# Performance work log

Measured on AMD Instinct MI355X. Metric: run time of the kernel, lower is better.

## Reference

```python
import jax, jax.numpy as jnp
import numpy as np

C_IN = 512


def _rms(h, gamma):
    # F.normalize(x, dim=1) * sqrt(C) * gamma  (channel_first, h: [b, c, l])
    c = h.shape[1]
    n = jnp.sqrt(jnp.sum(h * h, axis=1, keepdims=True))
    return h / jnp.maximum(n, 1e-12) * (c ** 0.5) * gamma[None, :, None]


def _pw(w, b, h):
    # 1x1 conv == pointwise linear over channel dim; h: [b, c, l]
    return jnp.einsum('oc,bcl->bol', w, h) + b[None, :, None]


def setup_inputs() -> dict:
    key = jax.random.key(0)
    ks = jax.random.split(key, 10)
    B, C, T, H, W = 1, C_IN, 16, 32, 32
    inp = {'x': jax.random.normal(ks[0], (B, C, T, H, W), jnp.float32)}
    names = ['qs', 'ks', 'vs', 'ps', 'qt', 'kt', 'vt', 'pt']
    for i, n in enumerate(names):
        inp[n + '_w'] = jax.random.normal(ks[i + 1], (C, C), jnp.float32) * 0.02
        inp[n + '_b'] = jnp.zeros((C,), jnp.float32)
    inp['norm_s_gamma'] = jnp.ones((C,), jnp.float32)
    inp['norm_t_gamma'] = jnp.ones((C,), jnp.float32)
    inp['max_temporal_window'] = 8
    return inp


def reference(x, qs_w, qs_b, ks_w, ks_b, vs_w, vs_b, ps_w, ps_b,
              qt_w, qt_b, kt_w, kt_b, vt_w, vt_b, pt_w, pt_b,
              norm_s_gamma, norm_t_gamma, max_temporal_window):
    B, C, T, H, W = x.shape
    scale = C ** -0.5

    # ---- spatial attention: (b t) c (h w) ----
    xs = x.transpose(0, 2, 1, 3, 4).reshape(B * T, C, H * W)
    h = _rms(xs, norm_s_gamma)
    q = _pw(qs_w, qs_b, h)
    k = _pw(ks_w, ks_b, h)
    v = _pw(vs_w, vs_b, h)
    scores = jnp.einsum('bcl,bcm->blm', q, k) * scale  # [bt, HW, HW]
    attn = jax.nn.softmax(scores, axis=-1)
    o = jnp.einsum('bcm,blm->bcl', v, attn)
    xs = xs + _pw(ps_w, ps_b, o)
    x = xs.reshape(B, T, C, H, W).transpose(0, 2, 1, 3, 4)

    # ---- temporal attention: (b h w) c t, causal + bounded window ----
    xt = x.transpose(0, 3, 4, 1, 2).reshape(B * H * W, C, T)
    h = _rms(xt, norm_t_gamma)
    q = _pw(qt_w, qt_b, h)
    k = _pw(kt_w, kt_b, h)
    v = _pw(vt_w, vt_b, h)
    scores = jnp.einsum('bcl,bcm->blm', q, k) * scale  # [bhw, T, T]
    i = jnp.arange(T)[:, None]
    j = jnp.arange(T)[None, :]
    allowed = j <= i  # causal
    if max_temporal_window is not None and max_temporal_window > 0:
        allowed = allowed & (i - j < max_temporal_window)  # sliding window
    mask = jnp.where(allowed, 0.0, jnp.finfo(scores.dtype).min)
    attn = jax.nn.softmax(scores + mask[None], axis=-1)
    o = jnp.einsum('bcm,blm->bcl', v, attn)
    xt = xt + _pw(pt_w, pt_b, o)
    x = xt.reshape(B, H, W, C, T).transpose(0, 3, 4, 1, 2)
    return x
```

## Files before the change

### kernel.cpp

```cpp
#include <hip/hip_runtime.h>

typedef __attribute__((ext_vector_type(8))) short bf16x8;
typedef __attribute__((ext_vector_type(4))) float f32x4;

__device__ __forceinline__ short f2bf(float f) {
  union { float f; unsigned u; } a; a.f = f;
  unsigned r = a.u + 0x7fffu + ((a.u >> 16) & 1u);
  return (short)(r >> 16);
}
__device__ __forceinline__ float bf2f(short s) {
  union { unsigned u; float f; } a;
  a.u = ((unsigned)(unsigned short)s) << 16; return a.f;
}
__device__ __forceinline__ float blo(unsigned u) { union { unsigned u; float f; } a; a.u = u << 16; return a.f; }
__device__ __forceinline__ float bhi(unsigned u) { union { unsigned u; float f; } a; a.u = u & 0xffff0000u; return a.f; }
__device__ __forceinline__ unsigned packbf(float lo, float hi) {
  return (unsigned)(unsigned short)f2bf(lo) | ((unsigned)(unsigned short)f2bf(hi) << 16);
}
__device__ __forceinline__ void ldscp16(const void* g, void* l) {
  __builtin_amdgcn_global_load_lds((const __attribute__((address_space(1))) void*)g,
                                   (__attribute__((address_space(3))) void*)l, 16, 0, 0);
}
__device__ __forceinline__ void stv(float* p, float v) { *p = v; }
__device__ __forceinline__ void stv(short* p, float v) { *p = f2bf(v); }

__global__ __launch_bounds__(256) void setup_all(
    const float* __restrict__ w0, const float* __restrict__ w1,
    const float* __restrict__ w2, const float* __restrict__ w3,
    const float* __restrict__ w4, const float* __restrict__ w5,
    const float* __restrict__ w6, const float* __restrict__ w7,
    const float* __restrict__ g_s, const float* __restrict__ g_t,
    short* __restrict__ Wb, float* __restrict__ zs,
    const float* __restrict__ qs_b, const float* __restrict__ vs_b,
    const float* __restrict__ ps_b, const float* __restrict__ qt_b,
    const float* __restrict__ vt_b, const float* __restrict__ pt_b,
    float* __restrict__ bt_s, float* __restrict__ bt_t,
    float* __restrict__ wus, float* __restrict__ wut) {
  const int bid = blockIdx.x, tid = threadIdx.x;
  if (bid < 8192) {
    int idx = bid * 256 + tid;
    const float* ws[8] = {w0, w1, w2, w3, w4, w5, w6, w7};
    int wi = idx >> 18, loc = idx & 262143;
    int r = loc >> 9, q = loc & 511;
    float v, g;
    if (wi == 3 || wi == 7) { v = ws[wi][loc]; g = 1.f; }
    else {
      v = ws[wi][q * 512 + r];
      g = (wi <= 2) ? g_s[r] : g_t[r];
    }
    Wb[idx] = f2bf(v * g);
  } else if (bid < 8512) {
    zs[(bid - 8192) * 256 + tid] = 0.f;
  } else {
    const int w = tid >> 6, lane = tid & 63;
    const int b = (bid - 8512) * 4 + w;
    float s = 0.f;
    if (b < 1024) {
      const bool sp = b < 512;
      const float* W = sp ? w3 : w7;
      const float* vb = sp ? vs_b : vt_b;
      const int r = b & 511;
#pragma unroll
      for (int c = lane; c < 512; c += 64) s += W[r * 512 + c] * vb[c];
#pragma unroll
      for (int off = 32; off > 0; off >>= 1) s += __shfl_xor(s, off);
      if (lane == 0) (sp ? bt_s : bt_t)[r] = s + (sp ? ps_b : pt_b)[r];
    } else {
      const bool sp = b < 1536;
      const float* W = sp ? w1 : w5;
      const float* qb = sp ? qs_b : qt_b;
      const int c = b & 511;
#pragma unroll
      for (int o = lane; o < 512; o += 64) s += W[o * 512 + c] * qb[o];
#pragma unroll
      for (int off = 32; off > 0; off >>= 1) s += __shfl_xor(s, off);
      if (lane == 0)
        (sp ? wus : wut)[c] = s * (sp ? g_s[c] : g_t[c]);
    }
  }
}

__global__ __launch_bounds__(256) void txp_sumsq(
    const float* __restrict__ src, short* __restrict__ dst,
    short* __restrict__ xb, float* __restrict__ ss,
    const float* __restrict__ wu, float* __restrict__ us) {
  constexpr long N = 16384;
  __shared__ short T[64][66];
  __shared__ float part[16][16][4];
  __shared__ float part2[16][16][4];
  const int tid = threadIdx.x;
  const long n0 = (long)blockIdx.x * 64;
  const int c0 = blockIdx.y * 64;
  const int n4 = (tid & 15) * 4;
  float s0 = 0.f, s1 = 0.f, s2 = 0.f, s3 = 0.f;
  float u0 = 0.f, u1 = 0.f, u2 = 0.f, u3 = 0.f;
#pragma unroll
  for (int i = 0; i < 4; ++i) {
    int cl = i * 16 + (tid >> 4);
    float4 v = *(const float4*)&src[(long)(c0 + cl) * N + n0 + n4];
    float wc = wu[c0 + cl];
    s0 += v.x * v.x; s1 += v.y * v.y; s2 += v.z * v.z; s3 += v.w * v.w;
    u0 += wc * v.x; u1 += wc * v.y; u2 += wc * v.z; u3 += wc * v.w;
    short e0 = f2bf(v.x), e1 = f2bf(v.y), e2 = f2bf(v.z), e3 = f2bf(v.w);
    T[n4 + 0][cl] = e0; T[n4 + 1][cl] = e1;
    T[n4 + 2][cl] = e2; T[n4 + 3][cl] = e3;
    uint2 o;
    o.x = (unsigned)(unsigned short)e0 | ((unsigned)(unsigned short)e1 << 16);
    o.y = (unsigned)(unsigned short)e2 | ((unsigned)(unsigned short)e3 << 16);
    *(uint2*)&xb[(long)(c0 + cl) * N + n0 + n4] = o;
  }
  part[tid >> 4][tid & 15][0] = s0; part[tid >> 4][tid & 15][1] = s1;
  part[tid >> 4][tid & 15][2] = s2; part[tid >> 4][tid & 15][3] = s3;
  part2[tid >> 4][tid & 15][0] = u0; part2[tid >> 4][tid & 15][1] = u1;
  part2[tid >> 4][tid & 15][2] = u2; part2[tid >> 4][tid & 15][3] = u3;
  __syncthreads();
  if (tid < 64) {
    float s = 0.f, u = 0.f;
#pragma unroll
    for (int cg = 0; cg < 16; ++cg) {
      s += part[cg][tid >> 2][tid & 3];
      u += part2[cg][tid >> 2][tid & 3];
    }
    atomicAdd(&ss[n0 + tid], s);
    atomicAdd(&us[n0 + tid], u);
  }
#pragma unroll
  for (int p = 0; p < 4; ++p) {
    int nl = p * 16 + (tid >> 4);
    int cl = (tid & 15) * 4;
    uint2 o;
    o.x = (unsigned)(unsigned short)T[nl][cl] |
          ((unsigned)(unsigned short)T[nl][cl + 1] << 16);
    o.y = (unsigned)(unsigned short)T[nl][cl + 2] |
          ((unsigned)(unsigned short)T[nl][cl + 3] << 16);
    *(uint2*)&dst[(n0 + nl) * 512 + c0 + cl] = o;
  }
}

template <typename OutT, int BIAS_MODE, int SCALE_MODE, int RESID_MODE, int EPI,
          int BM = 128, int FOLD = 0, int BK = 64>
__global__ __launch_bounds__(256, (BM == 128 && BK == 64) ? 3 : 2) void gemm_nt(
    const short* __restrict__ A, const short* __restrict__ B,
    OutT* __restrict__ D, const float* __restrict__ bias,
    const float* __restrict__ ssv, const float* __restrict__ uvec,
    float* __restrict__ rs, float* __restrict__ rs2,
    const float* __restrict__ wvec,
    const float* __restrict__ residf, const short* __restrict__ residb,
    int K, int lda, int ldb, int ldd,
    long aBatch, long bBatch, long dBatch, long sBatch, float scale) {
  constexpr int WR = BM / 64;
  constexpr int WC = 4 / WR;
  constexpr int NW = (128 / WC) / 16;
  constexpr int CH = BK / 8;
  constexpr int MSK = CH - 1;
  constexpr int RPR = 256 / CH;
  __shared__ short As[BM * BK];
  __shared__ short Bs[128 * BK];
  const int tid = threadIdx.x;
  const int bz = blockIdx.z;
  const long i0 = (long)blockIdx.x * BM;
  const long j0 = (long)blockIdx.y * 128;
  long aOff, bOff;
  if (FOLD) {
    aOff = 262144L * (bz < 2 ? 3 + 4 * bz : 4 * (bz - 2));
    bOff = 262144L * (bz < 2 ? 2 + 4 * bz : 1 + 4 * (bz - 2));
  } else {
    aOff = bz * aBatch; bOff = bz * bBatch;
  }
  const short* Ab = A + aOff + i0 * lda;
  const short* Bb = B + bOff + j0 * ldb;
  const int srow = tid / CH, scol = tid & MSK;
  const int lane = tid & 63;
  const int waveid = tid >> 6;
  const int wr = (waveid / WC) * 64;
  const int wc = (waveid % WC) * 64;
  const int quad = lane >> 4, l15 = lane & 15;

  f32x4 acc[4][NW] = {};

  for (int k0 = 0; k0 < K; k0 += BK) {
    __syncthreads();
#pragma unroll
    for (int p = 0; p < BM / RPR; ++p) {
      int row = p * RPR + srow;
      int gc = (scol ^ (row & MSK)) << 3;
      ldscp16(Ab + (long)row * lda + k0 + gc, &As[p * 2048 + tid * 8]);
    }
#pragma unroll
    for (int p = 0; p < 128 / RPR; ++p) {
      int row = p * RPR + srow;
      int gc = (scol ^ (row & MSK)) << 3;
      ldscp16(Bb + (long)row * ldb + k0 + gc, &Bs[p * 2048 + tid * 8]);
    }
    __syncthreads();
#pragma unroll
    for (int kk = 0; kk < BK / 32; ++kk) {
      bf16x8 af[4], bfr[NW];
#pragma unroll
      for (int a = 0; a < 4; ++a) {
        int row = wr + a * 16 + l15;
        int g = kk * 4 + quad;
        af[a] = *(const bf16x8*)&As[row * BK + ((g ^ (row & MSK)) << 3)];
      }
#pragma unroll
      for (int b = 0; b < NW; ++b) {
        int row = wc + b * 16 + l15;
        int g = kk * 4 + quad;
        bfr[b] = *(const bf16x8*)&Bs[row * BK + ((g ^ (row & MSK)) << 3)];
      }
#pragma unroll
      for (int a = 0; a < 4; ++a)
#pragma unroll
        for (int b = 0; b < NW; ++b)
          acc[a][b] = __builtin_amdgcn_mfma_f32_16x16x32_bf16(af[a], bfr[b], acc[a][b], 0, 0, 0);
    }
  }

  const long Doff = bz * dBatch;
#pragma unroll
  for (int a = 0; a < 4; ++a) {
    const int rb = (int)i0 + wr + a * 16 + quad * 4;
    float rsc[4];
    if (SCALE_MODE == 1 || SCALE_MODE == 4) {
#pragma unroll
      for (int r = 0; r < 4; ++r)
        rsc[r] = 22.627416997969522f /
                 fmaxf(sqrtf(ssv[bz * sBatch + rb + r]), 1e-12f);
    }
    if (SCALE_MODE == 3) {
#pragma unroll
      for (int r = 0; r < 4; ++r)
        rsc[r] = 1.f / ssv[bz * sBatch + rb + r];
    }
    float rp1[4] = {0.f, 0.f, 0.f, 0.f};
    float rp2[4] = {0.f, 0.f, 0.f, 0.f};
#pragma unroll
    for (int b = 0; b < NW; ++b) {
      const int cc = (int)j0 + wc + b * 16 + l15;
      float csc = 1.f, uu = 0.f, wv = 0.f;
      if (SCALE_MODE == 2 || SCALE_MODE == 4)
        csc = 22.627416997969522f /
              fmaxf(sqrtf(ssv[bz * sBatch + cc]), 1e-12f);
      if (SCALE_MODE == 4) uu = uvec[bz * sBatch + cc];
      if (EPI == 3) wv = wvec[cc];
      uint2 rtv;
      if (RESID_MODE == 3)
        rtv = *(const uint2*)&residb[(long)cc * 512 + rb];
#pragma unroll
      for (int r = 0; r < 4; ++r) {
        float val;
        if (SCALE_MODE == 4) {
          val = __expf(scale * csc * (rsc[r] * acc[a][b][r] + uu));
          rp1[r] += val;
          val *= csc;
        } else {
          val = acc[a][b][r] * scale;
          if (SCALE_MODE == 1 || SCALE_MODE == 3) val *= rsc[r];
          if (SCALE_MODE == 2) val *= csc;
        }
        if (BIAS_MODE == 1) val += bias[rb + r];
        if (BIAS_MODE == 2) val += bias[cc];
        const long off = Doff + (long)(rb + r) * ldd + cc;
        if (RESID_MODE == 1) val += residf[off];
        if (RESID_MODE == 2) val += bf2f(residb[off]);
        if (RESID_MODE == 3) val += bf2f(((const short*)&rtv)[r]);
        stv(D + off, val);
        if (EPI == 3) { rp1[r] += val * val; rp2[r] += val * wv; }
      }
    }
    if (EPI == 1 || EPI == 3) {
#pragma unroll
      for (int r = 0; r < 4; ++r) {
        float s = rp1[r];
#pragma unroll
        for (int off = 1; off < 16; off <<= 1) s += __shfl_xor(s, off);
        if (l15 == 0) atomicAdd(&rs[bz * sBatch + rb + r], s);
      }
      if (EPI == 3) {
#pragma unroll
        for (int r = 0; r < 4; ++r) {
          float s = rp2[r];
#pragma unroll
          for (int off = 1; off < 16; off <<= 1) s += __shfl_xor(s, off);
          if (l15 == 0) atomicAdd(&rs2[bz * sBatch + rb + r], s);
        }
      }
    }
  }
}

__global__ __launch_bounds__(256) void temporal_attn_v5(
    const short* __restrict__ h2, const short* __restrict__ Tt,
    const float* __restrict__ ss, const float* __restrict__ ut,
    const int* __restrict__ wndp, short* __restrict__ o, float scale) {
  constexpr int RS = 520;
  __shared__ short hq[16 * RS];
  __shared__ short tk[16 * RS];
  __shared__ float Plds[16][17];
  const int tid = threadIdx.x;
  const int w = tid >> 6, lane = tid & 63;
  const int hw = blockIdx.x;
  const int wnd = *wndp;

#pragma unroll
  for (int i = 0; i < 8; ++i) {
    int ci = w * 8 + i;
    int t = ci & 15;
    const short* src = (ci < 16) ? h2 : Tt;
    short* dst = (ci < 16) ? hq : tk;
    ldscp16(src + (long)(t * 1024 + hw) * 512 + lane * 8,
            dst + t * RS + lane * 8);
  }
  const int c0 = lane * 8;
  uint4 vch[16];
#pragma unroll
  for (int tp = 0; tp < 16; ++tp)
    vch[tp] = *(const uint4*)(h2 + (long)(tp * 1024 + hw) * 512 + c0);
  __syncthreads();

  if (w == 0) {
    const int quad = lane >> 4, m = lane & 15;
    f32x4 sacc = {};
#pragma unroll
    for (int s = 0; s < 16; ++s) {
      bf16x8 aq = *(const bf16x8*)&hq[m * RS + quad * 8 + s * 32];
      bf16x8 bk = *(const bf16x8*)&tk[m * RS + quad * 8 + s * 32];
      sacc = __builtin_amdgcn_mfma_f32_16x16x32_bf16(aq, bk, sacc, 0, 0, 0);
    }
    const float rmsj = 22.627416997969522f /
                       fmaxf(sqrtf(ss[m * 1024 + hw]), 1e-12f);
    const float uj = ut[m * 1024 + hw];
#pragma unroll
    for (int r = 0; r < 4; ++r) {
      const int i = quad * 4 + r;
      const int j = m;
      const float rmsi = 22.627416997969522f /
                         fmaxf(sqrtf(ss[i * 1024 + hw]), 1e-12f);
      const bool allowed = (j <= i) && (wnd <= 0 || (i - j) < wnd);
      float val = allowed ? scale * (rmsi * rmsj * sacc[r] + rmsj * uj) : -1e30f;
      float mx = val;
#pragma unroll
      for (int off = 1; off < 16; off <<= 1) mx = fmaxf(mx, __shfl_xor(mx, off));
      float e = allowed ? __expf(val - mx) : 0.f;
      float sum = e;
#pragma unroll
      for (int off = 1; off < 16; off <<= 1) sum += __shfl_xor(sum, off);
      Plds[i][j] = (e / sum) * rmsj;
    }
  }
  __syncthreads();

#pragma unroll
  for (int r = 0; r < 4; ++r) {
    const int t = w * 4 + r;
    const int tlo = (wnd > 0 && t - wnd + 1 > 0) ? t - wnd + 1 : 0;
    float a0 = 0.f, a1 = 0.f, a2 = 0.f, a3 = 0.f,
          a4 = 0.f, a5 = 0.f, a6 = 0.f, a7 = 0.f;
#pragma unroll
    for (int tp = 0; tp < 16; ++tp) {
      const float p = (tp >= tlo && tp <= t) ? Plds[t][tp] : 0.f;
      const uint4 vv = vch[tp];
      a0 += p * blo(vv.x); a1 += p * bhi(vv.x);
      a2 += p * blo(vv.y); a3 += p * bhi(vv.y);
      a4 += p * blo(vv.z); a5 += p * bhi(vv.z);
      a6 += p * blo(vv.w); a7 += p * bhi(vv.w);
    }
    uint4 ov;
    ov.x = packbf(a0, a1); ov.y = packbf(a2, a3);
    ov.z = packbf(a4, a5); ov.w = packbf(a6, a7);
    *(uint4*)(o + (long)(t * 1024 + hw) * 512 + c0) = ov;
  }
}

extern "C" void kernel_launch(void* const* d_in, const int* in_sizes, int n_in,
                              void* d_out, int out_size, void* d_ws, size_t ws_size,
                              hipStream_t stream) {
  const float* x    = (const float*)d_in[0];
  const float* qs_w = (const float*)d_in[1];
  const float* qs_b = (const float*)d_in[2];
  const float* ks_w = (const float*)d_in[3];
  const float* ks_b = (const float*)d_in[4];
  const float* vs_w = (const float*)d_in[5];
  const float* vs_b = (const float*)d_in[6];
  const float* ps_w = (const float*)d_in[7];
  const float* ps_b = (const float*)d_in[8];
  const float* qt_w = (const float*)d_in[9];
  const float* qt_b = (const float*)d_in[10];
  const float* kt_w = (const float*)d_in[11];
  const float* kt_b = (const float*)d_in[12];
  const float* vt_w = (const float*)d_in[13];
  const float* vt_b = (const float*)d_in[14];
  const float* pt_w = (const float*)d_in[15];
  const float* pt_b = (const float*)d_in[16];
  const float* g_s  = (const float*)d_in[17];
  const float* g_t  = (const float*)d_in[18];
  const int*   wnd  = (const int*)d_in[19];
  float* out = (float*)d_out;
  (void)ks_b; (void)kt_b;

  char* w = (char*)d_ws;
  short* Wb   = (short*)(w);
  float* ss_s = (float*)(w + (4L << 20));
  float* ss_t = (float*)(w + (4L << 20) + (64 << 10));
  float* rsum = (float*)(w + (4L << 20) + (128 << 10));
  float* us   = (float*)(w + (4L << 20) + (192 << 10));
  float* ut   = (float*)(w + (4L << 20) + (256 << 10));
  float* bt_s = (float*)(w + (4L << 20) + (320 << 10));
  float* bt_t = (float*)(w + (4L << 20) + (324 << 10));
  float* wus  = (float*)(w + (4L << 20) + (328 << 10));
  float* wut  = (float*)(w + (4L << 20) + (332 << 10));
  short* WF   = (short*)(w + (4L << 20) + (512 << 10));
  short* Wpv  = WF;
  short* Mqk  = WF + 2 * 262144;
  short* hb   = (short*)(w + (8L << 20));
  short* Tb   = (short*)(w + (24L << 20));
  short* xb   = (short*)(w + (40L << 20));
  short* oT   = (short*)(w + (56L << 20));
  short* h2   = (short*)(w + (72L << 20));
  short* S    = (short*)(w + (88L << 20));
  (void)in_sizes; (void)n_in; (void)out_size; (void)ws_size;

  const float scale = 0.04419417382415922f;

  setup_all<<<9024, 256, 0, stream>>>(
      qs_w, ks_w, vs_w, ps_w, qt_w, kt_w, vt_w, pt_w, g_s, g_t, Wb, ss_s,
      qs_b, vs_b, ps_b, qt_b, vt_b, pt_b, bt_s, bt_t, wus, wut);
  gemm_nt<short, 0, 0, 0, 0, 128, 1><<<dim3(4, 4, 4), 256, 0, stream>>>(
      Wb, Wb, WF, nullptr, nullptr, nullptr, nullptr, nullptr, nullptr,
      nullptr, nullptr, 512, 512, 512, 512, 0, 0, 262144L, 0, 1.f);

  txp_sumsq<<<dim3(256, 8, 1), 256, 0, stream>>>(x, hb, xb, ss_s, wus, us);
  gemm_nt<short, 0, 0, 0, 0, 128, 0, 128><<<dim3(128, 4, 1), 256, 0, stream>>>(
      hb, Mqk, Tb, nullptr, nullptr, nullptr, nullptr, nullptr, nullptr,
      nullptr, nullptr, 512, 512, 512, 512, 0, 0, 0, 0, 1.f);
  gemm_nt<short, 0, 4, 0, 1, 256><<<dim3(4, 8, 16), 256, 0, stream>>>(
      hb, Tb, S, nullptr, ss_s, us, rsum, nullptr, nullptr, nullptr, nullptr,
      512, 512, 512, 1024,
      1024L * 512, 1024L * 512, 1024L * 1024, 1024, scale);
  gemm_nt<short, 0, 3, 0, 0, 128, 0, 128><<<dim3(8, 4, 16), 256, 0, stream>>>(
      S, xb, oT, nullptr, rsum, nullptr, nullptr, nullptr, nullptr,
      nullptr, nullptr, 1024, 1024, 16384, 512,
      1024L * 1024, 1024L, 1024L * 512, 1024, 1.f);
  gemm_nt<short, 2, 0, 2, 3, 128, 0, 128><<<dim3(128, 4, 1), 256, 0, stream>>>(
      oT, Wpv, h2, bt_s, nullptr, nullptr, ss_t, ut, wut, nullptr, hb,
      512, 512, 512, 512, 0, 0, 0, 1024, 1.f);

  gemm_nt<short, 0, 0, 0, 0, 128, 0, 128><<<dim3(128, 4, 1), 256, 0, stream>>>(
      h2, Mqk + 262144, Tb, nullptr, nullptr, nullptr, nullptr, nullptr,
      nullptr, nullptr, nullptr, 512, 512, 512, 512, 0, 0, 0, 0, 1.f);
  temporal_attn_v5<<<1024, 256, 0, stream>>>(h2, Tb, ss_t, ut, wnd, oT, scale);
  gemm_nt<float, 1, 0, 3, 0, 128, 0, 128><<<dim3(4, 128, 1), 256, 0, stream>>>(
      Wpv + 262144, oT, out, bt_t, nullptr, nullptr, nullptr, nullptr,
      nullptr, nullptr, h2, 512, 512, 512, 16384, 0, 0, 0, 0, 1.f);
}
```

Before: 307.5 us.

## Double-buffer GEMM shared-memory tiles and unify tile shapes to BK=64

```diff
diff --git a/kernel.cpp b/kernel.cpp
--- a/kernel.cpp
+++ b/kernel.cpp
@@ -139,7 +139,7 @@
 
 template <typename OutT, int BIAS_MODE, int SCALE_MODE, int RESID_MODE, int EPI,
           int BM = 128, int FOLD = 0, int BK = 64>
-__global__ __launch_bounds__(256, (BM == 128 && BK == 64) ? 3 : 2) void gemm_nt(
+__global__ __launch_bounds__(256, 2) void gemm_nt(
     const short* __restrict__ A, const short* __restrict__ B,
     OutT* __restrict__ D, const float* __restrict__ bias,
     const float* __restrict__ ssv, const float* __restrict__ uvec,
@@ -154,8 +154,10 @@
   constexpr int CH = BK / 8;
   constexpr int MSK = CH - 1;
   constexpr int RPR = 256 / CH;
-  __shared__ short As[BM * BK];
-  __shared__ short Bs[128 * BK];
+  constexpr int ASZ = BM * BK;
+  constexpr int BSZ = 128 * BK;
+  __shared__ short As[2 * ASZ];
+  __shared__ short Bs[2 * BSZ];
   const int tid = threadIdx.x;
   const int bz = blockIdx.z;
   const long i0 = (long)blockIdx.x * BM;
@@ -178,21 +180,31 @@
 
   f32x4 acc[4][NW] = {};
 
-  for (int k0 = 0; k0 < K; k0 += BK) {
-    __syncthreads();
+  auto stage = [&](int buf, int k0) {
 #pragma unroll
     for (int p = 0; p < BM / RPR; ++p) {
       int row = p * RPR + srow;
       int gc = (scol ^ (row & MSK)) << 3;
-      ldscp16(Ab + (long)row * lda + k0 + gc, &As[p * 2048 + tid * 8]);
+      ldscp16(Ab + (long)row * lda + k0 + gc,
+              &As[buf * ASZ + p * 2048 + tid * 8]);
     }
 #pragma unroll
     for (int p = 0; p < 128 / RPR; ++p) {
       int row = p * RPR + srow;
       int gc = (scol ^ (row & MSK)) << 3;
-      ldscp16(Bb + (long)row * ldb + k0 + gc, &Bs[p * 2048 + tid * 8]);
-    }
-    __syncthreads();
+      ldscp16(Bb + (long)row * ldb + k0 + gc,
+              &Bs[buf * BSZ + p * 2048 + tid * 8]);
+    }
+  };
+
+  stage(0, 0);
+  __syncthreads();
+
+  int cur = 0;
+  for (int k0 = 0; k0 < K; k0 += BK) {
+    if (k0 + BK < K) stage(cur ^ 1, k0 + BK);
+    const short* Ar = &As[cur * ASZ];
+    const short* Br = &Bs[cur * BSZ];
 #pragma unroll
     for (int kk = 0; kk < BK / 32; ++kk) {
       bf16x8 af[4], bfr[NW];
@@ -200,13 +212,13 @@
       for (int a = 0; a < 4; ++a) {
         int row = wr + a * 16 + l15;
         int g = kk * 4 + quad;
-        af[a] = *(const bf16x8*)&As[row * BK + ((g ^ (row & MSK)) << 3)];
+        af[a] = *(const bf16x8*)&Ar[row * BK + ((g ^ (row & MSK)) << 3)];
       }
 #pragma unroll
       for (int b = 0; b < NW; ++b) {
         int row = wc + b * 16 + l15;
         int g = kk * 4 + quad;
-        bfr[b] = *(const bf16x8*)&Bs[row * BK + ((g ^ (row & MSK)) << 3)];
+        bfr[b] = *(const bf16x8*)&Br[row * BK + ((g ^ (row & MSK)) << 3)];
       }
 #pragma unroll
       for (int a = 0; a < 4; ++a)
@@ -214,6 +226,8 @@
         for (int b = 0; b < NW; ++b)
           acc[a][b] = __builtin_amdgcn_mfma_f32_16x16x32_bf16(af[a], bfr[b], acc[a][b], 0, 0, 0);
     }
+    __syncthreads();
+    cur ^= 1;
   }
 
   const long Doff = bz * dBatch;
@@ -430,26 +444,26 @@
       nullptr, nullptr, 512, 512, 512, 512, 0, 0, 262144L, 0, 1.f);
 
   txp_sumsq<<<dim3(256, 8, 1), 256, 0, stream>>>(x, hb, xb, ss_s, wus, us);
-  gemm_nt<short, 0, 0, 0, 0, 128, 0, 128><<<dim3(128, 4, 1), 256, 0, stream>>>(
+  gemm_nt<short, 0, 0, 0, 0, 128><<<dim3(128, 4, 1), 256, 0, stream>>>(
       hb, Mqk, Tb, nullptr, nullptr, nullptr, nullptr, nullptr, nullptr,
       nullptr, nullptr, 512, 512, 512, 512, 0, 0, 0, 0, 1.f);
-  gemm_nt<short, 0, 4, 0, 1, 256><<<dim3(4, 8, 16), 256, 0, stream>>>(
+  gemm_nt<short, 0, 4, 0, 1, 128><<<dim3(8, 8, 16), 256, 0, stream>>>(
       hb, Tb, S, nullptr, ss_s, us, rsum, nullptr, nullptr, nullptr, nullptr,
       512, 512, 512, 1024,
       1024L * 512, 1024L * 512, 1024L * 1024, 1024, scale);
-  gemm_nt<short, 0, 3, 0, 0, 128, 0, 128><<<dim3(8, 4, 16), 256, 0, stream>>>(
+  gemm_nt<short, 0, 3, 0, 0, 128><<<dim3(8, 4, 16), 256, 0, stream>>>(
       S, xb, oT, nullptr, rsum, nullptr, nullptr, nullptr, nullptr,
       nullptr, nullptr, 1024, 1024, 16384, 512,
       1024L * 1024, 1024L, 1024L * 512, 1024, 1.f);
-  gemm_nt<short, 2, 0, 2, 3, 128, 0, 128><<<dim3(128, 4, 1), 256, 0, stream>>>(
+  gemm_nt<short, 2, 0, 2, 3, 128><<<dim3(128, 4, 1), 256, 0, stream>>>(
       oT, Wpv, h2, bt_s, nullptr, nullptr, ss_t, ut, wut, nullptr, hb,
       512, 512, 512, 512, 0, 0, 0, 1024, 1.f);
 
-  gemm_nt<short, 0, 0, 0, 0, 128, 0, 128><<<dim3(128, 4, 1), 256, 0, stream>>>(
+  gemm_nt<short, 0, 0, 0, 0, 128><<<dim3(128, 4, 1), 256, 0, stream>>>(
       h2, Mqk + 262144, Tb, nullptr, nullptr, nullptr, nullptr, nullptr,
       nullptr, nullptr, nullptr, 512, 512, 512, 512, 0, 0, 0, 0, 1.f);
   temporal_attn_v5<<<1024, 256, 0, stream>>>(h2, Tb, ss_t, ut, wnd, oT, scale);
-  gemm_nt<float, 1, 0, 3, 0, 128, 0, 128><<<dim3(4, 128, 1), 256, 0, stream>>>(
+  gemm_nt<float, 1, 0, 3, 0, 128><<<dim3(4, 128, 1), 256, 0, stream>>>(
       Wpv + 262144, oT, out, bt_t, nullptr, nullptr, nullptr, nullptr,
       nullptr, nullptr, h2, 512, 512, 512, 16384, 0, 0, 0, 0, 1.f);
 }
```

New measurement: 306.9 us. Within noise of the previous version (-0.2%).

## Add XCD-aware block swizzle to GEMMs and switch to smaller K tiles

Applied to the files above, without the earlier changes.

```diff
diff --git a/kernel.cpp b/kernel.cpp
--- a/kernel.cpp
+++ b/kernel.cpp
@@ -138,8 +138,8 @@
 }
 
 template <typename OutT, int BIAS_MODE, int SCALE_MODE, int RESID_MODE, int EPI,
-          int BM = 128, int FOLD = 0, int BK = 64>
-__global__ __launch_bounds__(256, (BM == 128 && BK == 64) ? 3 : 2) void gemm_nt(
+          int BM = 128, int FOLD = 0, int BK = 64, int SWZ = 0>
+__global__ __launch_bounds__(256, 4) void gemm_nt(
     const short* __restrict__ A, const short* __restrict__ B,
     OutT* __restrict__ D, const float* __restrict__ bias,
     const float* __restrict__ ssv, const float* __restrict__ uvec,
@@ -157,9 +157,21 @@
   __shared__ short As[BM * BK];
   __shared__ short Bs[128 * BK];
   const int tid = threadIdx.x;
-  const int bz = blockIdx.z;
-  const long i0 = (long)blockIdx.x * BM;
-  const long j0 = (long)blockIdx.y * 128;
+
+  int lin = blockIdx.x + gridDim.x * (blockIdx.y + gridDim.y * blockIdx.z);
+  if (SWZ) {
+    const int nwg = gridDim.x * gridDim.y * gridDim.z;
+    const int q = nwg >> 3, r = nwg & 7;
+    const int xcd = lin & 7, idx = lin >> 3;
+    lin = (xcd < r ? xcd * (q + 1) : r * (q + 1) + (xcd - r) * q) + idx;
+  }
+  const int bx = lin % gridDim.x;
+  const int t1 = lin / gridDim.x;
+  const int by = t1 % gridDim.y;
+  const int bz = t1 / gridDim.y;
+
+  const long i0 = (long)bx * BM;
+  const long j0 = (long)by * 128;
   long aOff, bOff;
   if (FOLD) {
     aOff = 262144L * (bz < 2 ? 3 + 4 * bz : 4 * (bz - 2));
@@ -425,31 +437,31 @@
   setup_all<<<9024, 256, 0, stream>>>(
       qs_w, ks_w, vs_w, ps_w, qt_w, kt_w, vt_w, pt_w, g_s, g_t, Wb, ss_s,
       qs_b, vs_b, ps_b, qt_b, vt_b, pt_b, bt_s, bt_t, wus, wut);
-  gemm_nt<short, 0, 0, 0, 0, 128, 1><<<dim3(4, 4, 4), 256, 0, stream>>>(
+  gemm_nt<short, 0, 0, 0, 0, 128, 1, 64, 0><<<dim3(4, 4, 4), 256, 0, stream>>>(
       Wb, Wb, WF, nullptr, nullptr, nullptr, nullptr, nullptr, nullptr,
       nullptr, nullptr, 512, 512, 512, 512, 0, 0, 262144L, 0, 1.f);
 
   txp_sumsq<<<dim3(256, 8, 1), 256, 0, stream>>>(x, hb, xb, ss_s, wus, us);
-  gemm_nt<short, 0, 0, 0, 0, 128, 0, 128><<<dim3(128, 4, 1), 256, 0, stream>>>(
+  gemm_nt<short, 0, 0, 0, 0, 128, 0, 64, 1><<<dim3(128, 4, 1), 256, 0, stream>>>(
       hb, Mqk, Tb, nullptr, nullptr, nullptr, nullptr, nullptr, nullptr,
       nullptr, nullptr, 512, 512, 512, 512, 0, 0, 0, 0, 1.f);
-  gemm_nt<short, 0, 4, 0, 1, 256><<<dim3(4, 8, 16), 256, 0, stream>>>(
+  gemm_nt<short, 0, 4, 0, 1, 128, 0, 64, 1><<<dim3(8, 8, 16), 256, 0, stream>>>(
       hb, Tb, S, nullptr, ss_s, us, rsum, nullptr, nullptr, nullptr, nullptr,
       512, 512, 512, 1024,
       1024L * 512, 1024L * 512, 1024L * 1024, 1024, scale);
-  gemm_nt<short, 0, 3, 0, 0, 128, 0, 128><<<dim3(8, 4, 16), 256, 0, stream>>>(
+  gemm_nt<short, 0, 3, 0, 0, 128, 0, 64, 1><<<dim3(8, 4, 16), 256, 0, stream>>>(
       S, xb, oT, nullptr, rsum, nullptr, nullptr, nullptr, nullptr,
       nullptr, nullptr, 1024, 1024, 16384, 512,
       1024L * 1024, 1024L, 1024L * 512, 1024, 1.f);
-  gemm_nt<short, 2, 0, 2, 3, 128, 0, 128><<<dim3(128, 4, 1), 256, 0, stream>>>(
+  gemm_nt<short, 2, 0, 2, 3, 128, 0, 64, 1><<<dim3(128, 4, 1), 256, 0, stream>>>(
       oT, Wpv, h2, bt_s, nullptr, nullptr, ss_t, ut, wut, nullptr, hb,
       512, 512, 512, 512, 0, 0, 0, 1024, 1.f);
 
-  gemm_nt<short, 0, 0, 0, 0, 128, 0, 128><<<dim3(128, 4, 1), 256, 0, stream>>>(
+  gemm_nt<short, 0, 0, 0, 0, 128, 0, 64, 1><<<dim3(128, 4, 1), 256, 0, stream>>>(
       h2, Mqk + 262144, Tb, nullptr, nullptr, nullptr, nullptr, nullptr,
       nullptr, nullptr, nullptr, 512, 512, 512, 512, 0, 0, 0, 0, 1.f);
   temporal_attn_v5<<<1024, 256, 0, stream>>>(h2, Tb, ss_t, ut, wnd, oT, scale);
-  gemm_nt<float, 1, 0, 3, 0, 128, 0, 128><<<dim3(4, 128, 1), 256, 0, stream>>>(
+  gemm_nt<float, 1, 0, 3, 0, 128, 0, 64, 1><<<dim3(4, 128, 1), 256, 0, stream>>>(
       Wpv + 262144, oT, out, bt_t, nullptr, nullptr, nullptr, nullptr,
       nullptr, nullptr, h2, 512, 512, 512, 16384, 0, 0, 0, 0, 1.f);
 }
```

New measurement: 301.3 us. -2.0%, faster.
